# Performance work log

Hardware: AMD Instinct MI355X
Metric: run time of the kernel (lower is better)

Reference implementation:

```python
import jax, jax.numpy as jnp
import numpy as np

B, C, H, W = 16, 256, 32, 32
NUM_LAYERS = 30
OUT = 16  # sqrt(out_channels)
EPS = 1e-5


def setup_inputs() -> dict:
    key = jax.random.key(0)
    k1, k2, k3 = jax.random.split(key, 3)
    x = jax.random.normal(k1, (B, C, H, W), dtype=jnp.float32)
    # delta_t ~ small positive values (module inits ~N(0.01, 0.005))
    delta_t = jax.random.uniform(k2, (NUM_LAYERS, 1), dtype=jnp.float32) * 0.02
    matrices = jax.random.normal(k3, (NUM_LAYERS, 1, 1, OUT, OUT), dtype=jnp.float32) * 0.1
    gamma = jnp.ones((H * W,), dtype=jnp.float32)   # BatchNorm2d weight, oc = i*i = H*W
    beta = jnp.zeros((H * W,), dtype=jnp.float32)   # BatchNorm2d bias
    return {"x": x, "delta_t": delta_t, "matrices": matrices, "gamma": gamma, "beta": beta}


def _bn_relu6(z, gamma, beta):
    # training-mode BatchNorm2d over channel axis 1 (channels = H*W), then ReLU6
    mean = jnp.mean(z, axis=(0, 2, 3), keepdims=True)
    var = jnp.mean(jnp.square(z - mean), axis=(0, 2, 3), keepdims=True)  # biased var
    zhat = (z - mean) * jax.lax.rsqrt(var + EPS)
    g = gamma.reshape(1, -1, 1, 1)
    b = beta.reshape(1, -1, 1, 1)
    return jnp.clip(zhat * g + b, 0.0, 6.0)


def reference(x, delta_t, matrices, gamma, beta):
    b, c, h, w = x.shape
    hw = h * w
    # feature_reshape: [B,C,H,W] -> [B,HW,C] -> [B,HW,out,out] (inn == out branch)
    x1 = x.reshape(b, c, hw).transpose(0, 2, 1).reshape(b, hw, OUT, OUT)
    dt = jnp.clip(delta_t, 0.0, 6.0)[:, 0]  # relu6(delta_t), shape [L]

    def step(y0, params):
        m, dtl = params  # m: [1,1,out,out] broadcasts elementwise against x1
        dydt = -y0 + _bn_relu6(y0 + m * x1, gamma, beta)
        return y0 + dtl * dydt, None

    y0, _ = jax.lax.scan(step, x1, (matrices, dt))
    # (y0 + x1): [B, HW, out, out] -> view [B,H,W,out*out] -> permute to [B,out*out,H,W]
    y = (y0 + x1).reshape(b, h, w, OUT * OUT).transpose(0, 3, 1, 2)
    return y
```

## Files before the change

### kernel.cpp

```cpp
#include <hip/hip_runtime.h>

typedef float v2f __attribute__((ext_vector_type(2)));

#define HW      1024
#define NLAYERS 30
#define TPB     64

template <int CTRL, int RMASK>
__device__ __forceinline__ float dpp_add(float x) {
    int t = __builtin_amdgcn_update_dpp(0, __builtin_bit_cast(int, x),
                                        CTRL, RMASK, 0xf, true);
    return x + __builtin_bit_cast(float, t);
}
__device__ __forceinline__ float wave_sum64(float x) {
    x = dpp_add<0x111, 0xf>(x);
    x = dpp_add<0x112, 0xf>(x);
    x = dpp_add<0x114, 0xf>(x);
    x = dpp_add<0x118, 0xf>(x);
    x = dpp_add<0x142, 0xa>(x);
    x = dpp_add<0x143, 0xc>(x);
    return x;
}

__global__ __launch_bounds__(TPB, 1) void ode_wave(
    const float* __restrict__ x, const float* __restrict__ delta_t,
    const float* __restrict__ matrices, const float* __restrict__ gamma,
    const float* __restrict__ beta, float* __restrict__ out) {

    const int bid  = blockIdx.x;
    const int p    = ((bid & 7) << 7) | (bid >> 3);
    const int lane = threadIdx.x;

    v2f x1[4][8], y[4][8], z[4][8];
#pragma unroll
    for (int j = 0; j < 4; ++j) {
        const size_t base = (size_t)(lane + 64 * j) * HW + p;
#pragma unroll
        for (int i = 0; i < 8; ++i) {
            x1[j][i].x = x[base + (size_t)(2 * i)     * 256 * HW];
            x1[j][i].y = x[base + (size_t)(2 * i + 1) * 256 * HW];
            y[j][i] = x1[j][i];
        }
    }

    const float gp = gamma[p];
    const float bp = beta[p];

    float mn[4];
#pragma unroll
    for (int j = 0; j < 4; ++j) mn[j] = matrices[64 * j + lane];
    float dtn = delta_t[0];

    for (int lay = 0; lay < NLAYERS; ++lay) {
        const float dt = __builtin_amdgcn_fmed3f(dtn, 0.0f, 6.0f);
        v2f M[4];
#pragma unroll
        for (int j = 0; j < 4; ++j) { M[j].x = mn[j]; M[j].y = mn[j]; }

        const int nl = (lay < NLAYERS - 1) ? lay + 1 : lay;
#pragma unroll
        for (int j = 0; j < 4; ++j) mn[j] = matrices[nl * 256 + 64 * j + lane];
        dtn = delta_t[nl];

        v2f s[4], q[4];
#pragma unroll
        for (int j = 0; j < 4; ++j) {
            s[j] = (v2f){0.0f, 0.0f};
            q[j] = (v2f){0.0f, 0.0f};
        }
#pragma unroll
        for (int j = 0; j < 4; ++j) {
#pragma unroll
            for (int i = 0; i < 8; ++i) {
                const v2f zz = __builtin_elementwise_fma(M[j], x1[j][i], y[j][i]);
                z[j][i] = zz;
                s[j] += zz;
                q[j] = __builtin_elementwise_fma(zz, zz, q[j]);
            }
        }

        const v2f sv = (s[0] + s[1]) + (s[2] + s[3]);
        const v2f qv = (q[0] + q[1]) + (q[2] + q[3]);
        const float ssum = wave_sum64(sv.x + sv.y);
        const float qsum = wave_sum64(qv.x + qv.y);
        const float S = __shfl(ssum, 63, 64);
        const float Q = __shfl(qsum, 63, 64);

        const float mean = S * (1.0f / 4096.0f);
        const float var  = fmaf(-mean, mean, Q * (1.0f / 4096.0f));
        const float rstd = rsqrtf(var + 1e-5f);
        const float g    = gp * rstd;
        const float bb   = fmaf(-mean, g, bp);
        const v2f g2 = {g, g}, b2 = {bb, bb}, dt2 = {dt, dt};

#pragma unroll
        for (int j = 0; j < 4; ++j) {
#pragma unroll
            for (int i = 0; i < 8; ++i) {
                v2f a = __builtin_elementwise_fma(z[j][i], g2, b2);
                a.x = __builtin_amdgcn_fmed3f(a.x, 0.0f, 6.0f);
                a.y = __builtin_amdgcn_fmed3f(a.y, 0.0f, 6.0f);
                const v2f d = a - y[j][i];
                y[j][i] = __builtin_elementwise_fma(dt2, d, y[j][i]);
            }
        }
    }

#pragma unroll
    for (int j = 0; j < 4; ++j) {
        const size_t base = (size_t)(lane + 64 * j) * HW + p;
#pragma unroll
        for (int i = 0; i < 8; ++i) {
            out[base + (size_t)(2 * i)     * 256 * HW] = y[j][i].x + x1[j][i].x;
            out[base + (size_t)(2 * i + 1) * 256 * HW] = y[j][i].y + x1[j][i].y;
        }
    }
}

extern "C" void kernel_launch(void* const* d_in, const int* in_sizes, int n_in,
                              void* d_out, int out_size, void* d_ws, size_t ws_size,
                              hipStream_t stream) {
    const float* x        = (const float*)d_in[0];
    const float* delta_t  = (const float*)d_in[1];
    const float* matrices = (const float*)d_in[2];
    const float* gamma    = (const float*)d_in[3];
    const float* beta     = (const float*)d_in[4];
    float* out = (float*)d_out;

    ode_wave<<<dim3(HW), dim3(TPB), 0, stream>>>(x, delta_t, matrices, gamma, beta, out);
}
```

Measured before the change: 136.7 us.

## Split per-channel ODE across 8 waves with LDS reduction, two channels per block

Each block now handles two adjacent BN channels with 512 threads (8 waves), each thread owning 8 v2f elements instead of 64 floats. Batch statistics are reduced through a double-buffered LDS array plus one barrier per layer, and the update and next-layer statistics are fused into one pass. Loads and stores become 8-byte vectors over adjacent channels. This is meant to raise occupancy and memory coalescing and cut per-thread register pressure and serial latency. In exchange it adds a block-wide sync on every layer.

```diff
diff --git a/kernel.cpp b/kernel.cpp
--- a/kernel.cpp
+++ b/kernel.cpp
@@ -1,10 +1,11 @@
 #include <hip/hip_runtime.h>
 
 typedef float v2f __attribute__((ext_vector_type(2)));
+typedef float v4f __attribute__((ext_vector_type(4)));
 
 #define HW      1024
 #define NLAYERS 30
-#define TPB     64
+#define TPB     512
 
 template <int CTRL, int RMASK>
 __device__ __forceinline__ float dpp_add(float x) {
@@ -22,97 +23,115 @@
     return x;
 }
 
-__global__ __launch_bounds__(TPB, 1) void ode_wave(
+__global__ __launch_bounds__(TPB, 4) void ode2ch(
     const float* __restrict__ x, const float* __restrict__ delta_t,
     const float* __restrict__ matrices, const float* __restrict__ gamma,
     const float* __restrict__ beta, float* __restrict__ out) {
 
-    const int bid  = blockIdx.x;
-    const int p    = ((bid & 7) << 7) | (bid >> 3);
-    const int lane = threadIdx.x;
+    const int bid = blockIdx.x;
+    const int gs  = ((bid & 7) << 6) | (bid >> 3);
+    const int p0  = gs << 1;
+    const int t   = threadIdx.x;
+    const int c   = t & 255;
+    const int bb0 = t >> 8;
+    const int wid = t >> 6;
+    const int lane = t & 63;
 
-    v2f x1[4][8], y[4][8], z[4][8];
+    __shared__ v4f red[2][8];
+
+    v2f x1[8], y[8], z[8];
 #pragma unroll
-    for (int j = 0; j < 4; ++j) {
-        const size_t base = (size_t)(lane + 64 * j) * HW + p;
+    for (int i = 0; i < 8; ++i) {
+        const size_t off = (size_t)((2 * i + bb0) * 256 + c) * HW + p0;
+        x1[i] = *(const v2f*)(x + off);
+        y[i]  = x1[i];
+    }
+
+    const v2f gp2 = *(const v2f*)(gamma + p0);
+    const v2f bp2 = *(const v2f*)(beta + p0);
+
+    {
+        const float m0 = matrices[c];
+        const v2f M0 = {m0, m0};
+        v2f s = {0.f, 0.f}, q = {0.f, 0.f};
 #pragma unroll
         for (int i = 0; i < 8; ++i) {
-            x1[j][i].x = x[base + (size_t)(2 * i)     * 256 * HW];
-            x1[j][i].y = x[base + (size_t)(2 * i + 1) * 256 * HW];
-            y[j][i] = x1[j][i];
+            z[i] = __builtin_elementwise_fma(M0, x1[i], y[i]);
+            s += z[i];
+            q = __builtin_elementwise_fma(z[i], z[i], q);
         }
+        const float sx = wave_sum64(s.x), sy = wave_sum64(s.y);
+        const float qx = wave_sum64(q.x), qy = wave_sum64(q.y);
+        if (lane == 63) { v4f w; w.x = sx; w.y = sy; w.z = qx; w.w = qy; red[0][wid] = w; }
     }
 
-    const float gp = gamma[p];
-    const float bp = beta[p];
+    float m_cur  = matrices[256 + c];
+    float dt_cur = delta_t[0];
+    float dt_nxt = delta_t[1];
+    __syncthreads();
 
-    float mn[4];
+    for (int k = 0; k < NLAYERS - 1; ++k) {
+        const int k2 = (k + 2 < NLAYERS) ? k + 2 : NLAYERS - 1;
+        const float m_nxt  = matrices[k2 * 256 + c];
+        const float dt_nn  = delta_t[k2];
+
+        const v4f* r = red[k & 1];
+        v4f a0 = r[0] + r[1], a1 = r[2] + r[3], a2 = r[4] + r[5], a3 = r[6] + r[7];
+        const v4f acc = (a0 + a1) + (a2 + a3);
+
+        const float dtk = __builtin_amdgcn_fmed3f(dt_cur, 0.0f, 6.0f);
+        const v2f mean2 = {acc.x * (1.0f / 4096.0f), acc.y * (1.0f / 4096.0f)};
+        const v2f msq2  = {acc.z * (1.0f / 4096.0f), acc.w * (1.0f / 4096.0f)};
+        const v2f var2  = __builtin_elementwise_fma(-mean2, mean2, msq2);
+        v2f rstd; rstd.x = rsqrtf(var2.x + 1e-5f); rstd.y = rsqrtf(var2.y + 1e-5f);
+        const v2f g2 = gp2 * rstd;
+        const v2f b2 = __builtin_elementwise_fma(-mean2, g2, bp2);
+        const v2f dt2 = {dtk, dtk};
+        const v2f M2  = {m_cur, m_cur};
+
+        v2f s = {0.f, 0.f}, q = {0.f, 0.f};
 #pragma unroll
-    for (int j = 0; j < 4; ++j) mn[j] = matrices[64 * j + lane];
-    float dtn = delta_t[0];
+        for (int i = 0; i < 8; ++i) {
+            v2f a = __builtin_elementwise_fma(z[i], g2, b2);
+            a.x = __builtin_amdgcn_fmed3f(a.x, 0.0f, 6.0f);
+            a.y = __builtin_amdgcn_fmed3f(a.y, 0.0f, 6.0f);
+            const v2f d = a - y[i];
+            y[i] = __builtin_elementwise_fma(dt2, d, y[i]);
+            z[i] = __builtin_elementwise_fma(M2, x1[i], y[i]);
+            s += z[i];
+            q = __builtin_elementwise_fma(z[i], z[i], q);
+        }
+        const float sx = wave_sum64(s.x), sy = wave_sum64(s.y);
+        const float qx = wave_sum64(q.x), qy = wave_sum64(q.y);
+        if (lane == 63) { v4f w; w.x = sx; w.y = sy; w.z = qx; w.w = qy; red[(k + 1) & 1][wid] = w; }
 
-    for (int lay = 0; lay < NLAYERS; ++lay) {
-        const float dt = __builtin_amdgcn_fmed3f(dtn, 0.0f, 6.0f);
-        v2f M[4];
-#pragma unroll
-        for (int j = 0; j < 4; ++j) { M[j].x = mn[j]; M[j].y = mn[j]; }
+        m_cur = m_nxt; dt_cur = dt_nxt; dt_nxt = dt_nn;
+        __syncthreads();
+    }
 
-        const int nl = (lay < NLAYERS - 1) ? lay + 1 : lay;
-#pragma unroll
-        for (int j = 0; j < 4; ++j) mn[j] = matrices[nl * 256 + 64 * j + lane];
-        dtn = delta_t[nl];
+    {
+        const v4f* r = red[(NLAYERS - 1) & 1];
+        v4f a0 = r[0] + r[1], a1 = r[2] + r[3], a2 = r[4] + r[5], a3 = r[6] + r[7];
+        const v4f acc = (a0 + a1) + (a2 + a3);
 
-        v2f s[4], q[4];
-#pragma unroll
-        for (int j = 0; j < 4; ++j) {
-            s[j] = (v2f){0.0f, 0.0f};
-            q[j] = (v2f){0.0f, 0.0f};
-        }
-#pragma unroll
-        for (int j = 0; j < 4; ++j) {
-#pragma unroll
-            for (int i = 0; i < 8; ++i) {
-                const v2f zz = __builtin_elementwise_fma(M[j], x1[j][i], y[j][i]);
-                z[j][i] = zz;
-                s[j] += zz;
-                q[j] = __builtin_elementwise_fma(zz, zz, q[j]);
-            }
-        }
-
-        const v2f sv = (s[0] + s[1]) + (s[2] + s[3]);
-        const v2f qv = (q[0] + q[1]) + (q[2] + q[3]);
-        const float ssum = wave_sum64(sv.x + sv.y);
-        const float qsum = wave_sum64(qv.x + qv.y);
-        const float S = __shfl(ssum, 63, 64);
-        const float Q = __shfl(qsum, 63, 64);
-
-        const float mean = S * (1.0f / 4096.0f);
-        const float var  = fmaf(-mean, mean, Q * (1.0f / 4096.0f));
-        const float rstd = rsqrtf(var + 1e-5f);
-        const float g    = gp * rstd;
-        const float bb   = fmaf(-mean, g, bp);
-        const v2f g2 = {g, g}, b2 = {bb, bb}, dt2 = {dt, dt};
+        const float dtk = __builtin_amdgcn_fmed3f(dt_cur, 0.0f, 6.0f);
+        const v2f mean2 = {acc.x * (1.0f / 4096.0f), acc.y * (1.0f / 4096.0f)};
+        const v2f msq2  = {acc.z * (1.0f / 4096.0f), acc.w * (1.0f / 4096.0f)};
+        const v2f var2  = __builtin_elementwise_fma(-mean2, mean2, msq2);
+        v2f rstd; rstd.x = rsqrtf(var2.x + 1e-5f); rstd.y = rsqrtf(var2.y + 1e-5f);
+        const v2f g2 = gp2 * rstd;
+        const v2f b2 = __builtin_elementwise_fma(-mean2, g2, bp2);
+        const v2f dt2 = {dtk, dtk};
 
 #pragma unroll
-        for (int j = 0; j < 4; ++j) {
-#pragma unroll
-            for (int i = 0; i < 8; ++i) {
-                v2f a = __builtin_elementwise_fma(z[j][i], g2, b2);
-                a.x = __builtin_amdgcn_fmed3f(a.x, 0.0f, 6.0f);
-                a.y = __builtin_amdgcn_fmed3f(a.y, 0.0f, 6.0f);
-                const v2f d = a - y[j][i];
-                y[j][i] = __builtin_elementwise_fma(dt2, d, y[j][i]);
-            }
-        }
-    }
-
-#pragma unroll
-    for (int j = 0; j < 4; ++j) {
-        const size_t base = (size_t)(lane + 64 * j) * HW + p;
-#pragma unroll
         for (int i = 0; i < 8; ++i) {
-            out[base + (size_t)(2 * i)     * 256 * HW] = y[j][i].x + x1[j][i].x;
-            out[base + (size_t)(2 * i + 1) * 256 * HW] = y[j][i].y + x1[j][i].y;
+            v2f a = __builtin_elementwise_fma(z[i], g2, b2);
+            a.x = __builtin_amdgcn_fmed3f(a.x, 0.0f, 6.0f);
+            a.y = __builtin_amdgcn_fmed3f(a.y, 0.0f, 6.0f);
+            const v2f d = a - y[i];
+            const v2f yf = __builtin_elementwise_fma(dt2, d, y[i]);
+            const size_t off = (size_t)((2 * i + bb0) * 256 + c) * HW + p0;
+            *(v2f*)(out + off) = yf + x1[i];
         }
     }
 }
@@ -127,5 +146,5 @@
     const float* beta     = (const float*)d_in[4];
     float* out = (float*)d_out;
 
-    ode_wave<<<dim3(HW), dim3(TPB), 0, stream>>>(x, delta_t, matrices, gamma, beta, out);
+    ode2ch<<<dim3(HW / 2), dim3(TPB), 0, stream>>>(x, delta_t, matrices, gamma, beta, out);
 }
```

Measured after the change: 123.0 us. 1.11x faster.

## Spread each BN channel across 512 threads with LDS double-buffered reductions

Applied to the files above, without the earlier changes.

Moves each channel's 4096 elements from one 64-lane wave holding 64 values per lane to a 512-thread block holding 8 values per thread. The per-layer reduction now combines eight wave sums through a double-buffered shared array with one barrier per layer. The loop is also reordered so the normalize/update of layer k is fused with the sum pass of layer k+1, and packed FP32 ops are emitted through inline asm. This raises occupancy and latency hiding, at the cost of a block-wide barrier and LDS traffic on every layer.

```diff
diff --git a/kernel.cpp b/kernel.cpp
--- a/kernel.cpp
+++ b/kernel.cpp
@@ -1,10 +1,24 @@
 #include <hip/hip_runtime.h>
 
 typedef float v2f __attribute__((ext_vector_type(2)));
+typedef float v4f __attribute__((ext_vector_type(4)));
 
 #define HW      1024
 #define NLAYERS 30
-#define TPB     64
+#define TPB     512
+
+static __device__ __forceinline__ v2f pk_fma(v2f a, v2f b, v2f c) {
+    v2f d; asm("v_pk_fma_f32 %0, %1, %2, %3" : "=v"(d) : "v"(a), "v"(b), "v"(c));
+    return d;
+}
+static __device__ __forceinline__ v2f pk_add(v2f a, v2f b) {
+    v2f d; asm("v_pk_add_f32 %0, %1, %2" : "=v"(d) : "v"(a), "v"(b));
+    return d;
+}
+static __device__ __forceinline__ v2f pk_mul(v2f a, v2f b) {
+    v2f d; asm("v_pk_mul_f32 %0, %1, %2" : "=v"(d) : "v"(a), "v"(b));
+    return d;
+}
 
 template <int CTRL, int RMASK>
 __device__ __forceinline__ float dpp_add(float x) {
@@ -22,97 +36,123 @@
     return x;
 }
 
-__global__ __launch_bounds__(TPB, 1) void ode_wave(
+__global__ __launch_bounds__(TPB, 8) void ode_hiocc(
     const float* __restrict__ x, const float* __restrict__ delta_t,
     const float* __restrict__ matrices, const float* __restrict__ gamma,
     const float* __restrict__ beta, float* __restrict__ out) {
 
     const int bid  = blockIdx.x;
     const int p    = ((bid & 7) << 7) | (bid >> 3);
-    const int lane = threadIdx.x;
+    const int t    = threadIdx.x;
+    const int c    = t & 255;
+    const int wid  = t >> 6;
+    const int lane = t & 63;
 
-    v2f x1[4][8], y[4][8], z[4][8];
+    __shared__ __align__(16) v2f red[2][8];
+
+    v2f x1[4], y[4], z[4];
 #pragma unroll
     for (int j = 0; j < 4; ++j) {
-        const size_t base = (size_t)(lane + 64 * j) * HW + p;
-#pragma unroll
-        for (int i = 0; i < 8; ++i) {
-            x1[j][i].x = x[base + (size_t)(2 * i)     * 256 * HW];
-            x1[j][i].y = x[base + (size_t)(2 * i + 1) * 256 * HW];
-            y[j][i] = x1[j][i];
-        }
+        const uint32_t e0 = (uint32_t)t + 512u * j;
+        x1[j].x = x[(size_t)e0 * HW + p];
+        x1[j].y = x[(size_t)(e0 + 2048u) * HW + p];
+        y[j] = x1[j];
     }
 
     const float gp = gamma[p];
     const float bp = beta[p];
 
-    float mn[4];
-#pragma unroll
-    for (int j = 0; j < 4; ++j) mn[j] = matrices[64 * j + lane];
-    float dtn = delta_t[0];
-
-    for (int lay = 0; lay < NLAYERS; ++lay) {
-        const float dt = __builtin_amdgcn_fmed3f(dtn, 0.0f, 6.0f);
-        v2f M[4];
-#pragma unroll
-        for (int j = 0; j < 4; ++j) { M[j].x = mn[j]; M[j].y = mn[j]; }
-
-        const int nl = (lay < NLAYERS - 1) ? lay + 1 : lay;
-#pragma unroll
-        for (int j = 0; j < 4; ++j) mn[j] = matrices[nl * 256 + 64 * j + lane];
-        dtn = delta_t[nl];
-
-        v2f s[4], q[4];
+    {
+        const float m0 = matrices[c];
+        const v2f M0 = {m0, m0};
+        v2f s = {0.f, 0.f}, q = {0.f, 0.f};
 #pragma unroll
         for (int j = 0; j < 4; ++j) {
-            s[j] = (v2f){0.0f, 0.0f};
-            q[j] = (v2f){0.0f, 0.0f};
+            z[j] = pk_fma(M0, x1[j], y[j]);
+            s = pk_add(s, z[j]);
+            q = pk_fma(z[j], z[j], q);
         }
-#pragma unroll
-        for (int j = 0; j < 4; ++j) {
-#pragma unroll
-            for (int i = 0; i < 8; ++i) {
-                const v2f zz = __builtin_elementwise_fma(M[j], x1[j][i], y[j][i]);
-                z[j][i] = zz;
-                s[j] += zz;
-                q[j] = __builtin_elementwise_fma(zz, zz, q[j]);
-            }
-        }
+        const float ss = wave_sum64(s.x + s.y);
+        const float qq = wave_sum64(q.x + q.y);
+        if (lane == 63) red[0][wid] = (v2f){ss, qq};
+    }
 
-        const v2f sv = (s[0] + s[1]) + (s[2] + s[3]);
-        const v2f qv = (q[0] + q[1]) + (q[2] + q[3]);
-        const float ssum = wave_sum64(sv.x + sv.y);
-        const float qsum = wave_sum64(qv.x + qv.y);
-        const float S = __shfl(ssum, 63, 64);
-        const float Q = __shfl(qsum, 63, 64);
+    float m_cur  = matrices[256 + c];
+    float dt_cur = delta_t[0];
+    float dt_nxt = delta_t[1];
+    __syncthreads();
 
+    for (int k = 0; k < NLAYERS - 1; ++k) {
+        const int k2 = (k + 2 < NLAYERS) ? k + 2 : NLAYERS - 1;
+        const float m_nxt = matrices[k2 * 256 + c];
+        const float dt_nn = delta_t[k2];
+
+        const int par = k & 1;
+        const v4f* r = (const v4f*)&red[par][0];
+        const v4f u0 = r[0] + r[1], u1 = r[2] + r[3];
+        const v4f u = u0 + u1;
+        const float S = u.x + u.z;
+        const float Q = u.y + u.w;
+
+        const float dtk  = __builtin_amdgcn_fmed3f(dt_cur, 0.0f, 6.0f);
         const float mean = S * (1.0f / 4096.0f);
         const float var  = fmaf(-mean, mean, Q * (1.0f / 4096.0f));
         const float rstd = rsqrtf(var + 1e-5f);
         const float g    = gp * rstd;
-        const float bb   = fmaf(-mean, g, bp);
-        const v2f g2 = {g, g}, b2 = {bb, bb}, dt2 = {dt, dt};
+        const float b    = fmaf(-mean, g, bp);
+        const v2f g2 = {g, g}, b2 = {b, b};
+        const v2f dt2 = {dtk, dtk};
+        const v2f om2 = {1.0f - dtk, 1.0f - dtk};
+        const v2f M2  = {m_cur, m_cur};
+
+        v2f s = {0.f, 0.f}, q = {0.f, 0.f};
+#pragma unroll
+        for (int j = 0; j < 4; ++j) {
+            v2f a = pk_fma(z[j], g2, b2);
+            a.x = __builtin_amdgcn_fmed3f(a.x, 0.0f, 6.0f);
+            a.y = __builtin_amdgcn_fmed3f(a.y, 0.0f, 6.0f);
+            y[j] = pk_mul(om2, y[j]);
+            y[j] = pk_fma(dt2, a, y[j]);
+            z[j] = pk_fma(M2, x1[j], y[j]);
+            s = pk_add(s, z[j]);
+            q = pk_fma(z[j], z[j], q);
+        }
+        const float ss = wave_sum64(s.x + s.y);
+        const float qq = wave_sum64(q.x + q.y);
+        if (lane == 63) red[par ^ 1][wid] = (v2f){ss, qq};
+
+        m_cur = m_nxt; dt_cur = dt_nxt; dt_nxt = dt_nn;
+        __syncthreads();
+    }
+
+    {
+        const v4f* r = (const v4f*)&red[(NLAYERS - 1) & 1][0];
+        const v4f u0 = r[0] + r[1], u1 = r[2] + r[3];
+        const v4f u = u0 + u1;
+        const float S = u.x + u.z;
+        const float Q = u.y + u.w;
+
+        const float dtk  = __builtin_amdgcn_fmed3f(dt_cur, 0.0f, 6.0f);
+        const float mean = S * (1.0f / 4096.0f);
+        const float var  = fmaf(-mean, mean, Q * (1.0f / 4096.0f));
+        const float rstd = rsqrtf(var + 1e-5f);
+        const float g    = gp * rstd;
+        const float b    = fmaf(-mean, g, bp);
+        const v2f g2 = {g, g}, b2 = {b, b};
+        const v2f dt2 = {dtk, dtk};
+        const v2f om2 = {1.0f - dtk, 1.0f - dtk};
 
 #pragma unroll
         for (int j = 0; j < 4; ++j) {
-#pragma unroll
-            for (int i = 0; i < 8; ++i) {
-                v2f a = __builtin_elementwise_fma(z[j][i], g2, b2);
-                a.x = __builtin_amdgcn_fmed3f(a.x, 0.0f, 6.0f);
-                a.y = __builtin_amdgcn_fmed3f(a.y, 0.0f, 6.0f);
-                const v2f d = a - y[j][i];
-                y[j][i] = __builtin_elementwise_fma(dt2, d, y[j][i]);
-            }
-        }
-    }
-
-#pragma unroll
-    for (int j = 0; j < 4; ++j) {
-        const size_t base = (size_t)(lane + 64 * j) * HW + p;
-#pragma unroll
-        for (int i = 0; i < 8; ++i) {
-            out[base + (size_t)(2 * i)     * 256 * HW] = y[j][i].x + x1[j][i].x;
-            out[base + (size_t)(2 * i + 1) * 256 * HW] = y[j][i].y + x1[j][i].y;
+            v2f a = pk_fma(z[j], g2, b2);
+            a.x = __builtin_amdgcn_fmed3f(a.x, 0.0f, 6.0f);
+            a.y = __builtin_amdgcn_fmed3f(a.y, 0.0f, 6.0f);
+            y[j] = pk_mul(om2, y[j]);
+            y[j] = pk_fma(dt2, a, y[j]);
+            const v2f o = pk_add(y[j], x1[j]);
+            const uint32_t e0 = (uint32_t)t + 512u * j;
+            out[(size_t)e0 * HW + p]           = o.x;
+            out[(size_t)(e0 + 2048u) * HW + p] = o.y;
         }
     }
 }
@@ -127,5 +167,5 @@
     const float* beta     = (const float*)d_in[4];
     float* out = (float*)d_out;
 
-    ode_wave<<<dim3(HW), dim3(TPB), 0, stream>>>(x, delta_t, matrices, gamma, beta, out);
+    ode_hiocc<<<dim3(HW), dim3(TPB), 0, stream>>>(x, delta_t, matrices, gamma, beta, out);
 }
```

Measured after the change: 136.8 us. About the same (+0.1%).
